# Optimization experiments

Hardware: AMD Instinct MI355X
Metric: run time of the kernel (lower is better)

Reference implementation:

```python
import jax, jax.numpy as jnp
import numpy as np

B, S, D = 2, 2048, 1024
H = 16
DH = D // H
FF = 4096
N_NEU = 4096
N_PAT = 64
K = 16          # neuron top-k
KP = 8          # pattern top-k
EPS = 1e-5


def _layer_norm(x, g, b):
    mu = jnp.mean(x, axis=-1, keepdims=True)
    var = jnp.mean((x - mu) ** 2, axis=-1, keepdims=True)
    return (x - mu) * jax.lax.rsqrt(var + EPS) * g + b


def setup_inputs() -> dict:
    key = jax.random.key(0)
    ks = jax.random.split(key, 20)
    sc = 0.02
    lin = lambda k, o, i: jax.random.normal(k, (o, i), jnp.float32) * (1.0 / np.sqrt(i))
    return {
        "x": jax.random.normal(ks[0], (B, S, D), jnp.float32),
        "neurons": jax.random.normal(ks[1], (N_NEU, D), jnp.float32) * sc,
        "wq": lin(ks[2], D, D), "bq": jnp.zeros((D,), jnp.float32),
        "wk": lin(ks[3], D, D), "bk": jnp.zeros((D,), jnp.float32),
        "wv": lin(ks[4], D, D), "bv": jnp.zeros((D,), jnp.float32),
        "wp": lin(ks[5], 2, 2 * D), "bp": jnp.zeros((2,), jnp.float32),
        "pattern_queries": jax.random.normal(ks[6], (N_PAT, D), jnp.float32) * sc,
        "gates": jax.random.normal(ks[7], (N_PAT, FF), jnp.float32) * sc,
        "w_up": lin(ks[8], FF, D), "b_up": jnp.zeros((FF,), jnp.float32),
        "w_down": lin(ks[9], D, FF), "b_down": jnp.zeros((D,), jnp.float32),
        "ln1_g": jnp.ones((D,), jnp.float32), "ln1_b": jnp.zeros((D,), jnp.float32),
        "ln2_g": jnp.ones((D,), jnp.float32), "ln2_b": jnp.zeros((D,), jnp.float32),
    }


def _forward(x, neurons, wq, bq, wk, bk, wv, bv, wp, bp, pattern_queries, gates,
             w_up, b_up, w_down, b_down, ln1_g, ln1_b, ln2_g, ln2_b):
    # ---- NeuronRouter on norm1(x) ----
    normed = _layer_norm(x, ln1_g, ln1_b)
    q = (normed @ wq.T + bq).reshape(B, S, H, DH).transpose(0, 2, 1, 3)
    k = (normed @ wk.T + bk).reshape(B, S, H, DH).transpose(0, 2, 1, 3)
    v = (normed @ wv.T + bv).reshape(B, S, H, DH).transpose(0, 2, 1, 3)
    attn = jax.nn.softmax(jnp.einsum('bhqd,bhkd->bhqk', q, k) / np.sqrt(DH), axis=-1)
    context = jnp.einsum('bhqk,bhkd->bhqd', attn, v).transpose(0, 2, 1, 3).reshape(B, S, D)

    token_scores = normed @ neurons.T                     # [B,S,N]
    context_scores = context @ neurons.T                  # [B,S,N]
    combined = jnp.concatenate([normed, context], axis=-1)
    path_w = jax.nn.softmax(combined @ wp.T + bp, axis=-1)  # [B,S,2]
    scores = path_w[..., 0:1] * token_scores + path_w[..., 1:2] * context_scores

    topk_scores, topk_idx = jax.lax.top_k(scores, K)      # [B,S,K]
    topk_weights = jax.nn.softmax(topk_scores, axis=-1)
    selected = neurons[topk_idx]                          # [B,S,K,D]
    router_out = jnp.einsum('bsk,bskd->bsd', topk_weights, selected)

    x = x + router_out

    # ---- PatternFFN on norm2(x) ----
    normed2 = _layer_norm(x, ln2_g, ln2_b)
    # similarity * neuron weight, summed over K -> pattern scores [B,S,P]
    pattern_scores = jnp.einsum('pd,bskd,bsk->bsp', pattern_queries, selected,
                                topk_weights) / np.sqrt(D)
    pat_scores, pat_idx = jax.lax.top_k(pattern_scores, KP)  # [B,S,KP]
    pat_weights = jax.nn.softmax(pat_scores, axis=-1)
    selected_gates = gates[pat_idx]                       # [B,S,KP,FF]
    ffn_gate = jnp.einsum('bsk,bskf->bsf', pat_weights, selected_gates)

    h = normed2 @ w_up.T + b_up                           # [B,S,FF]
    h = jax.nn.gelu(h * jax.nn.sigmoid(ffn_gate), approximate=False)
    ffn_out = h @ w_down.T + b_down

    return x + ffn_out, topk_idx


def reference(x, neurons, wq, bq, wk, bk, wv, bv, wp, bp, pattern_queries, gates,
              w_up, b_up, w_down, b_down, ln1_g, ln1_b, ln2_g, ln2_b):
    return _forward(x, neurons, wq, bq, wk, bk, wv, bv, wp, bp, pattern_queries,
                    gates, w_up, b_up, w_down, b_down, ln1_g, ln1_b, ln2_g, ln2_b)
```

## Files before the change

kernel.cpp:

```cpp
#include <hip/hip_runtime.h>
#include <math.h>

#define DEV static __device__ __forceinline__

constexpr int S_ = 2048;
constexpr int D_ = 1024;
constexpr int H_ = 16;

typedef __attribute__((ext_vector_type(8))) short bf16x8;
typedef __attribute__((ext_vector_type(4))) float f32x4;
typedef __attribute__((ext_vector_type(8))) short s16x8;

DEV unsigned short f2bf(float x) {
    union { float f; unsigned u; } c; c.f = x;
    const unsigned r = (c.u + 0x7FFFu + ((c.u >> 16) & 1u)) >> 16;
    return (unsigned short)r;
}
DEV float bf2f(unsigned short u) {
    union { unsigned u; float f; } c; c.u = ((unsigned)u) << 16;
    return c.f;
}

DEV float blockReduceSum(float v) {
    #pragma unroll
    for (int m = 1; m < 64; m <<= 1) v += __shfl_xor(v, m, 64);
    __shared__ float wsr[4];
    const int lane = threadIdx.x & 63, wid = threadIdx.x >> 6;
    if (lane == 0) wsr[wid] = v;
    __syncthreads();
    v = wsr[0] + wsr[1] + wsr[2] + wsr[3];
    __syncthreads();
    return v;
}

template<int BF16OUT>
__global__ __launch_bounds__(256)
void ln_k(const float* __restrict__ x, const float* __restrict__ g,
          const float* __restrict__ b, void* __restrict__ o)
{
    const int m = blockIdx.x, tid = threadIdx.x;
    const float* xr = x + (size_t)m * D_;
    const float4 xv = *(const float4*)(xr + tid * 4);
    float s = xv.x + xv.y + xv.z + xv.w;
    s = blockReduceSum(s);
    const float mu = s * (1.0f / 1024.0f);
    const float d0 = xv.x - mu, d1 = xv.y - mu, d2 = xv.z - mu, d3 = xv.w - mu;
    float sq = d0 * d0 + d1 * d1 + d2 * d2 + d3 * d3;
    sq = blockReduceSum(sq);
    const float rstd = rsqrtf(sq * (1.0f / 1024.0f) + 1e-5f);
    const float4 gv = *(const float4*)(g + tid * 4);
    const float4 bv = *(const float4*)(b + tid * 4);
    const float o0 = d0 * rstd * gv.x + bv.x;
    const float o1 = d1 * rstd * gv.y + bv.y;
    const float o2 = d2 * rstd * gv.z + bv.z;
    const float o3 = d3 * rstd * gv.w + bv.w;
    if constexpr (BF16OUT) {
        unsigned short* ob = (unsigned short*)o + (size_t)m * D_ + tid * 4;
        *(ushort4*)ob = make_ushort4(f2bf(o0), f2bf(o1), f2bf(o2), f2bf(o3));
    } else {
        *(float4*)((float*)o + (size_t)m * D_ + tid * 4) = make_float4(o0, o1, o2, o3);
    }
}

template<int MODE>
__global__ __launch_bounds__(256)
void gemm32_k(const float* __restrict__ A, const float* __restrict__ Bw,
              const float* __restrict__ bias, const float* __restrict__ extra,
              float* __restrict__ Cout, int M, int N, int Kd)
{
    __shared__ __align__(16) float As[32][132];
    __shared__ __align__(16) float Bs[32][132];
    const int tid = threadIdx.x;
    const int tx = tid & 15, ty = tid >> 4;
    const int row0 = blockIdx.y * 128, col0 = blockIdx.x * 128;
    const int lr = tid & 127, lk = (tid >> 7) * 16;
    const float* Ap = A + (size_t)(row0 + lr) * Kd + lk;
    const float* Bp = Bw + (size_t)(col0 + lr) * Kd + lk;
    float acc[8][8] = {};

    float4 ar[4], br[4];
    #pragma unroll
    for (int jj = 0; jj < 4; ++jj) {
        ar[jj] = *(const float4*)(Ap + jj * 4);
        br[jj] = *(const float4*)(Bp + jj * 4);
    }

    for (int k0 = 0; k0 < Kd; k0 += 32) {
        __syncthreads();
        #pragma unroll
        for (int jj = 0; jj < 4; ++jj) {
            As[lk + jj * 4 + 0][lr] = ar[jj].x;
            As[lk + jj * 4 + 1][lr] = ar[jj].y;
            As[lk + jj * 4 + 2][lr] = ar[jj].z;
            As[lk + jj * 4 + 3][lr] = ar[jj].w;
            Bs[lk + jj * 4 + 0][lr] = br[jj].x;
            Bs[lk + jj * 4 + 1][lr] = br[jj].y;
            Bs[lk + jj * 4 + 2][lr] = br[jj].z;
            Bs[lk + jj * 4 + 3][lr] = br[jj].w;
        }
        __syncthreads();
        if (k0 + 32 < Kd) {
            #pragma unroll
            for (int jj = 0; jj < 4; ++jj) {
                ar[jj] = *(const float4*)(Ap + k0 + 32 + jj * 4);
                br[jj] = *(const float4*)(Bp + k0 + 32 + jj * 4);
            }
        }
        #pragma unroll
        for (int kk = 0; kk < 32; ++kk) {
            float av[8], bv[8];
            *(float4*)&av[0] = *(const float4*)&As[kk][ty * 8];
            *(float4*)&av[4] = *(const float4*)&As[kk][ty * 8 + 4];
            *(float4*)&bv[0] = *(const float4*)&Bs[kk][tx * 8];
            *(float4*)&bv[4] = *(const float4*)&Bs[kk][tx * 8 + 4];
            #pragma unroll
            for (int r = 0; r < 8; ++r)
                #pragma unroll
                for (int c = 0; c < 8; ++c)
                    acc[r][c] = fmaf(av[r], bv[c], acc[r][c]);
        }
    }

    const int gr0 = row0 + ty * 8, gc0 = col0 + tx * 8;
    if constexpr (MODE == 0) {
        const int hh = gc0 >> 6, dh = gc0 & 63;
        const float4 bias0 = *(const float4*)(bias + gc0);
        const float4 bias1 = *(const float4*)(bias + gc0 + 4);
        #pragma unroll
        for (int r = 0; r < 8; ++r) {
            const int m = gr0 + r;
            const int bb = m >> 11, s = m & (S_ - 1);
            float* dst = Cout + (((size_t)(bb * H_ + hh) * S_ + s) * 64 + dh);
            *(float4*)dst = make_float4(acc[r][0] + bias0.x, acc[r][1] + bias0.y,
                                        acc[r][2] + bias0.z, acc[r][3] + bias0.w);
            *(float4*)(dst + 4) = make_float4(acc[r][4] + bias1.x, acc[r][5] + bias1.y,
                                              acc[r][6] + bias1.z, acc[r][7] + bias1.w);
        }
    } else if constexpr (MODE == 2) {
        #pragma unroll
        for (int r = 0; r < 8; ++r) {
            const float rs = extra[2 * (gr0 + r)];
            float* dst = Cout + (size_t)(gr0 + r) * N + gc0;
            *(float4*)dst = make_float4(rs * acc[r][0], rs * acc[r][1],
                                        rs * acc[r][2], rs * acc[r][3]);
            *(float4*)(dst + 4) = make_float4(rs * acc[r][4], rs * acc[r][5],
                                              rs * acc[r][6], rs * acc[r][7]);
        }
    } else {
        #pragma unroll
        for (int r = 0; r < 8; ++r) {
            const float rs = extra[2 * (gr0 + r)];
            float* dst = Cout + (size_t)(gr0 + r) * N + gc0;
            const float4 c0 = *(const float4*)dst;
            const float4 c1 = *(const float4*)(dst + 4);
            *(float4*)dst = make_float4(c0.x + rs * acc[r][0], c0.y + rs * acc[r][1],
                                        c0.z + rs * acc[r][2], c0.w + rs * acc[r][3]);
            *(float4*)(dst + 4) = make_float4(c1.x + rs * acc[r][4], c1.y + rs * acc[r][5],
                                              c1.z + rs * acc[r][6], c1.w + rs * acc[r][7]);
        }
    }
}

__global__ __launch_bounds__(256)
void attn3_k(const float* __restrict__ q, const float* __restrict__ k,
             const float* __restrict__ v, float* __restrict__ ctx)
{
    __shared__ __align__(16) float Qs[64][68];
    __shared__ __align__(16) float Ks[64][68];
    __shared__ __align__(16) float Vs[64][68];
    __shared__ __align__(16) float Ps[64][68];
    const int tid = threadIdx.x;
    const int tx = tid & 15, ty = tid >> 4;
    const int bh = blockIdx.y;
    const int q0 = blockIdx.x * 64;
    const float* qb = q + (size_t)bh * S_ * 64;
    const float* kb = k + (size_t)bh * S_ * 64;
    const float* vb = v + (size_t)bh * S_ * 64;

    const int j = tid & 63, dc = (tid >> 6) * 16;

    {
        const float* src = qb + (size_t)(q0 + j) * 64 + dc;
        const float4 t0 = *(const float4*)(src + 0);
        const float4 t1 = *(const float4*)(src + 4);
        const float4 t2 = *(const float4*)(src + 8);
        const float4 t3 = *(const float4*)(src + 12);
        Qs[dc + 0][j] = t0.x;  Qs[dc + 1][j] = t0.y;  Qs[dc + 2][j] = t0.z;  Qs[dc + 3][j] = t0.w;
        Qs[dc + 4][j] = t1.x;  Qs[dc + 5][j] = t1.y;  Qs[dc + 6][j] = t1.z;  Qs[dc + 7][j] = t1.w;
        Qs[dc + 8][j] = t2.x;  Qs[dc + 9][j] = t2.y;  Qs[dc + 10][j] = t2.z; Qs[dc + 11][j] = t2.w;
        Qs[dc + 12][j] = t3.x; Qs[dc + 13][j] = t3.y; Qs[dc + 14][j] = t3.z; Qs[dc + 15][j] = t3.w;
    }

    float4 kr0, kr1, kr2, kr3, vr0, vr1, vr2, vr3;
    {
        const float* ks = kb + (size_t)j * 64 + dc;
        const float* vs = vb + (size_t)j * 64 + dc;
        kr0 = *(const float4*)(ks + 0);  kr1 = *(const float4*)(ks + 4);
        kr2 = *(const float4*)(ks + 8);  kr3 = *(const float4*)(ks + 12);
        vr0 = *(const float4*)(vs + 0);  vr1 = *(const float4*)(vs + 4);
        vr2 = *(const float4*)(vs + 8);  vr3 = *(const float4*)(vs + 12);
    }

    float mrow[4] = {-INFINITY, -INFINITY, -INFINITY, -INFINITY};
    float lrow[4] = {0.f, 0.f, 0.f, 0.f};
    float acc[4][4] = {};

    for (int kt = 0; kt < S_; kt += 64) {
        __syncthreads();
        Ks[dc + 0][j] = kr0.x;  Ks[dc + 1][j] = kr0.y;  Ks[dc + 2][j] = kr0.z;  Ks[dc + 3][j] = kr0.w;
        Ks[dc + 4][j] = kr1.x;  Ks[dc + 5][j] = kr1.y;  Ks[dc + 6][j] = kr1.z;  Ks[dc + 7][j] = kr1.w;
        Ks[dc + 8][j] = kr2.x;  Ks[dc + 9][j] = kr2.y;  Ks[dc + 10][j] = kr2.z; Ks[dc + 11][j] = kr2.w;
        Ks[dc + 12][j] = kr3.x; Ks[dc + 13][j] = kr3.y; Ks[dc + 14][j] = kr3.z; Ks[dc + 15][j] = kr3.w;
        *(float4*)&Vs[j][dc + 0]  = vr0;
        *(float4*)&Vs[j][dc + 4]  = vr1;
        *(float4*)&Vs[j][dc + 8]  = vr2;
        *(float4*)&Vs[j][dc + 12] = vr3;
        __syncthreads();

        if (kt + 64 < S_) {
            const float* ks = kb + (size_t)(kt + 64 + j) * 64 + dc;
            const float* vs = vb + (size_t)(kt + 64 + j) * 64 + dc;
            kr0 = *(const float4*)(ks + 0);  kr1 = *(const float4*)(ks + 4);
            kr2 = *(const float4*)(ks + 8);  kr3 = *(const float4*)(ks + 12);
            vr0 = *(const float4*)(vs + 0);  vr1 = *(const float4*)(vs + 4);
            vr2 = *(const float4*)(vs + 8);  vr3 = *(const float4*)(vs + 12);
        }

        float s[4][4] = {};
        #pragma unroll 8
        for (int d = 0; d < 64; ++d) {
            const float4 q4 = *(const float4*)&Qs[d][ty * 4];
            const float4 k4 = *(const float4*)&Ks[d][tx * 4];
            s[0][0] = fmaf(q4.x, k4.x, s[0][0]); s[0][1] = fmaf(q4.x, k4.y, s[0][1]);
            s[0][2] = fmaf(q4.x, k4.z, s[0][2]); s[0][3] = fmaf(q4.x, k4.w, s[0][3]);
            s[1][0] = fmaf(q4.y, k4.x, s[1][0]); s[1][1] = fmaf(q4.y, k4.y, s[1][1]);
            s[1][2] = fmaf(q4.y, k4.z, s[1][2]); s[1][3] = fmaf(q4.y, k4.w, s[1][3]);
            s[2][0] = fmaf(q4.z, k4.x, s[2][0]); s[2][1] = fmaf(q4.z, k4.y, s[2][1]);
            s[2][2] = fmaf(q4.z, k4.z, s[2][2]); s[2][3] = fmaf(q4.z, k4.w, s[2][3]);
            s[3][0] = fmaf(q4.w, k4.x, s[3][0]); s[3][1] = fmaf(q4.w, k4.y, s[3][1]);
            s[3][2] = fmaf(q4.w, k4.z, s[3][2]); s[3][3] = fmaf(q4.w, k4.w, s[3][3]);
        }

        #pragma unroll
        for (int r = 0; r < 4; ++r) {
            float s0 = s[r][0] * 0.125f, s1 = s[r][1] * 0.125f;
            float s2 = s[r][2] * 0.125f, s3 = s[r][3] * 0.125f;
            float rm = fmaxf(fmaxf(s0, s1), fmaxf(s2, s3));
            #pragma unroll
            for (int sh = 1; sh < 16; sh <<= 1) rm = fmaxf(rm, __shfl_xor(rm, sh, 64));
            const float mn = fmaxf(mrow[r], rm);
            const float p0 = expf(s0 - mn), p1 = expf(s1 - mn);
            const float p2 = expf(s2 - mn), p3 = expf(s3 - mn);
            float rs = p0 + p1 + p2 + p3;
            #pragma unroll
            for (int sh = 1; sh < 16; sh <<= 1) rs += __shfl_xor(rs, sh, 64);
            const float esc = expf(mrow[r] - mn);
            lrow[r] = lrow[r] * esc + rs;
            mrow[r] = mn;
            acc[r][0] *= esc; acc[r][1] *= esc; acc[r][2] *= esc; acc[r][3] *= esc;
            *(float4*)&Ps[ty * 4 + r][tx * 4] = make_float4(p0, p1, p2, p3);
        }
        __syncthreads();

        #pragma unroll 4
        for (int jb = 0; jb < 16; ++jb) {
            const float4 v0 = *(const float4*)&Vs[jb * 4 + 0][tx * 4];
            const float4 v1 = *(const float4*)&Vs[jb * 4 + 1][tx * 4];
            const float4 v2 = *(const float4*)&Vs[jb * 4 + 2][tx * 4];
            const float4 v3 = *(const float4*)&Vs[jb * 4 + 3][tx * 4];
            #pragma unroll
            for (int r = 0; r < 4; ++r) {
                const float4 p4 = *(const float4*)&Ps[ty * 4 + r][jb * 4];
                acc[r][0] = fmaf(p4.x, v0.x, acc[r][0]); acc[r][1] = fmaf(p4.x, v0.y, acc[r][1]);
                acc[r][2] = fmaf(p4.x, v0.z, acc[r][2]); acc[r][3] = fmaf(p4.x, v0.w, acc[r][3]);
                acc[r][0] = fmaf(p4.y, v1.x, acc[r][0]); acc[r][1] = fmaf(p4.y, v1.y, acc[r][1]);
                acc[r][2] = fmaf(p4.y, v1.z, acc[r][2]); acc[r][3] = fmaf(p4.y, v1.w, acc[r][3]);
                acc[r][0] = fmaf(p4.z, v2.x, acc[r][0]); acc[r][1] = fmaf(p4.z, v2.y, acc[r][1]);
                acc[r][2] = fmaf(p4.z, v2.z, acc[r][2]); acc[r][3] = fmaf(p4.z, v2.w, acc[r][3]);
                acc[r][0] = fmaf(p4.w, v3.x, acc[r][0]); acc[r][1] = fmaf(p4.w, v3.y, acc[r][1]);
                acc[r][2] = fmaf(p4.w, v3.z, acc[r][2]); acc[r][3] = fmaf(p4.w, v3.w, acc[r][3]);
            }
        }
    }

    const int bb = bh >> 4, hh = bh & 15;
    #pragma unroll
    for (int r = 0; r < 4; ++r) {
        const float inv = 1.0f / lrow[r];
        *(float4*)(ctx + (size_t)(bb * S_ + q0 + ty * 4 + r) * D_ + hh * 64 + tx * 4) =
            make_float4(acc[r][0] * inv, acc[r][1] * inv, acc[r][2] * inv, acc[r][3] * inv);
    }
}

__global__ __launch_bounds__(256)
void pathw_k(const float* __restrict__ normed, const float* __restrict__ ctx,
             const float* __restrict__ wp, const float* __restrict__ bp,
             float* __restrict__ pw)
{
    const int m = blockIdx.x, tid = threadIdx.x;
    const float4 n4 = *(const float4*)(normed + (size_t)m * D_ + tid * 4);
    const float4 c4 = *(const float4*)(ctx + (size_t)m * D_ + tid * 4);
    const float4 w0n = *(const float4*)(wp + tid * 4);
    const float4 w0c = *(const float4*)(wp + 1024 + tid * 4);
    const float4 w1n = *(const float4*)(wp + 2048 + tid * 4);
    const float4 w1c = *(const float4*)(wp + 3072 + tid * 4);
    float p0 = n4.x * w0n.x + n4.y * w0n.y + n4.z * w0n.z + n4.w * w0n.w
             + c4.x * w0c.x + c4.y * w0c.y + c4.z * w0c.z + c4.w * w0c.w;
    float p1 = n4.x * w1n.x + n4.y * w1n.y + n4.z * w1n.z + n4.w * w1n.w
             + c4.x * w1c.x + c4.y * w1c.y + c4.z * w1c.z + c4.w * w1c.w;
    p0 = blockReduceSum(p0);
    p1 = blockReduceSum(p1);
    if (tid == 0) {
        const float l0 = p0 + bp[0], l1 = p1 + bp[1];
        const float mx = fmaxf(l0, l1);
        const float e0 = expf(l0 - mx), e1 = expf(l1 - mx);
        const float inv = 1.0f / (e0 + e1);
        pw[2 * m] = e0 * inv;
        pw[2 * m + 1] = e1 * inv;
    }
}

__global__ __launch_bounds__(256)
void topk_router_k(const float* __restrict__ scores, const float* __restrict__ neurons,
                   const float* __restrict__ x, float* __restrict__ idx_out,
                   float* __restrict__ x1, float* __restrict__ router)
{
    __shared__ __align__(16) float sc[4096];
    __shared__ unsigned long long wred[4];
    __shared__ int ki_s[16];
    __shared__ float kv_s[16];
    __shared__ float kw_s[16];
    const int m = blockIdx.x, tid = threadIdx.x;
    const float* srow = scores + (size_t)m * 4096;
    for (int i = tid; i < 1024; i += 256)
        *(float4*)&sc[i * 4] = *(const float4*)(srow + i * 4);
    __syncthreads();

    for (int t = 0; t < 16; ++t) {
        unsigned long long best = 0ull;
        for (int i = tid; i < 4096; i += 256) {
            unsigned u = __float_as_uint(sc[i]);
            u = (u & 0x80000000u) ? ~u : (u | 0x80000000u);
            const unsigned long long key =
                ((unsigned long long)u << 32) | (unsigned long long)(0xFFFFFFFFu - (unsigned)i);
            if (key > best) best = key;
        }
        #pragma unroll
        for (int sh = 1; sh < 64; sh <<= 1) {
            const unsigned long long o = __shfl_xor(best, sh, 64);
            if (o > best) best = o;
        }
        if ((tid & 63) == 0) wred[tid >> 6] = best;
        __syncthreads();
        if (tid == 0) {
            unsigned long long bb = wred[0];
            if (wred[1] > bb) bb = wred[1];
            if (wred[2] > bb) bb = wred[2];
            if (wred[3] > bb) bb = wred[3];
            const int idx = (int)(0xFFFFFFFFu - (unsigned)(bb & 0xFFFFFFFFull));
            ki_s[t] = idx;
            kv_s[t] = sc[idx];
            sc[idx] = -INFINITY;
        }
        __syncthreads();
    }

    if (tid == 0) {
        const float mx = kv_s[0];
        float es[16], sum = 0.f;
        #pragma unroll
        for (int t = 0; t < 16; ++t) { es[t] = expf(kv_s[t] - mx); sum += es[t]; }
        const float inv = 1.0f / sum;
        #pragma unroll
        for (int t = 0; t < 16; ++t) kw_s[t] = es[t] * inv;
    }
    __syncthreads();

    if (tid < 16) idx_out[(size_t)m * 16 + tid] = (float)ki_s[tid];

    float4 r = make_float4(0.f, 0.f, 0.f, 0.f);
    #pragma unroll
    for (int t = 0; t < 16; ++t) {
        const float w = kw_s[t];
        const float4 nv = *(const float4*)(neurons + (size_t)ki_s[t] * D_ + tid * 4);
        r.x = fmaf(w, nv.x, r.x); r.y = fmaf(w, nv.y, r.y);
        r.z = fmaf(w, nv.z, r.z); r.w = fmaf(w, nv.w, r.w);
    }
    const float4 xv = *(const float4*)(x + (size_t)m * D_ + tid * 4);
    *(float4*)(router + (size_t)m * D_ + tid * 4) = r;
    *(float4*)(x1 + (size_t)m * D_ + tid * 4) =
        make_float4(xv.x + r.x, xv.y + r.y, xv.z + r.z, xv.w + r.w);
}

__global__ __launch_bounds__(256)
void pattern_k(const float* __restrict__ router, const float* __restrict__ pq,
               const float* __restrict__ gates, unsigned short* __restrict__ gate_out)
{
    __shared__ __align__(16) float rr[1024];
    __shared__ float ps[64];
    __shared__ int pidx[8];
    __shared__ float pwt[8];
    const int m = blockIdx.x, tid = threadIdx.x;
    *(float4*)&rr[tid * 4] = *(const float4*)(router + (size_t)m * D_ + tid * 4);
    __syncthreads();

    const int p = tid >> 2, part = tid & 3;
    const float* pqr = pq + (size_t)p * D_ + part * 256;
    float sum = 0.f;
    for (int d = 0; d < 256; d += 4) {
        const float4 a = *(const float4*)(pqr + d);
        const float4 b = *(const float4*)&rr[part * 256 + d];
        sum += a.x * b.x + a.y * b.y + a.z * b.z + a.w * b.w;
    }
    sum += __shfl_xor(sum, 1, 64);
    sum += __shfl_xor(sum, 2, 64);
    if (part == 0) ps[p] = sum * (1.0f / 32.0f);
    __syncthreads();

    if (tid == 0) {
        float kv[8];
        for (int t = 0; t < 8; ++t) {
            float bv = -INFINITY; int bi = 0;
            for (int i = 0; i < 64; ++i) {
                const float vv = ps[i];
                if (vv > bv) { bv = vv; bi = i; }
            }
            kv[t] = bv; pidx[t] = bi; ps[bi] = -INFINITY;
        }
        const float mx = kv[0];
        float ee[8], tot = 0.f;
        for (int t = 0; t < 8; ++t) { ee[t] = expf(kv[t] - mx); tot += ee[t]; }
        for (int t = 0; t < 8; ++t) pwt[t] = ee[t] / tot;
    }
    __syncthreads();

    for (int f = tid * 4; f < 4096; f += 1024) {
        float4 g = make_float4(0.f, 0.f, 0.f, 0.f);
        #pragma unroll
        for (int t = 0; t < 8; ++t) {
            const float w = pwt[t];
            const float4 gv = *(const float4*)(gates + (size_t)pidx[t] * 4096 + f);
            g.x = fmaf(w, gv.x, g.x); g.y = fmaf(w, gv.y, g.y);
            g.z = fmaf(w, gv.z, g.z); g.w = fmaf(w, gv.w, g.w);
        }
        *(ushort4*)(gate_out + (size_t)m * 4096 + f) =
            make_ushort4(f2bf(g.x), f2bf(g.y), f2bf(g.z), f2bf(g.w));
    }
}

__global__ __launch_bounds__(256)
void castbf_k(const float* __restrict__ in, unsigned short* __restrict__ out, int n)
{
    const int i = (blockIdx.x * 256 + threadIdx.x) * 8;
    if (i >= n) return;
    const float4 a = *(const float4*)(in + i);
    const float4 b = *(const float4*)(in + i + 4);
    *(ushort4*)(out + i) = make_ushort4(f2bf(a.x), f2bf(a.y), f2bf(a.z), f2bf(a.w));
    *(ushort4*)(out + i + 4) = make_ushort4(f2bf(b.x), f2bf(b.y), f2bf(b.z), f2bf(b.w));
}

template<int EPI>
__global__ __launch_bounds__(256)
void gemmbf_k(const unsigned short* __restrict__ A, const unsigned short* __restrict__ Bw,
              const float* __restrict__ bias, const unsigned short* __restrict__ gate,
              const float* resid, void* Cout, int M, int N, int Kd)
{
    constexpr int LSH = 40;
    __shared__ __align__(16) unsigned short Al[128 * LSH];
    __shared__ __align__(16) unsigned short Bl[128 * LSH];
    const int tid = threadIdx.x;
    const int lane = tid & 63;
    const int w = tid >> 6, wr = w >> 1, wc = w & 1;
    const int row0 = blockIdx.y * 128, col0 = blockIdx.x * 128;

    const int o0 = tid * 16, o1 = o0 + 4096;
    const int r0 = o0 >> 6, k0e = (o0 & 63) >> 1;
    const int r1 = o1 >> 6, k1e = (o1 & 63) >> 1;
    const int l0 = r0 * LSH + k0e, l1 = r1 * LSH + k1e;
    const unsigned short* Ap0 = A + (size_t)(row0 + r0) * Kd + k0e;
    const unsigned short* Ap1 = A + (size_t)(row0 + r1) * Kd + k1e;
    const unsigned short* Bp0 = Bw + (size_t)(col0 + r0) * Kd + k0e;
    const unsigned short* Bp1 = Bw + (size_t)(col0 + r1) * Kd + k1e;

    f32x4 acc[4][4];
    #pragma unroll
    for (int m = 0; m < 4; ++m)
        #pragma unroll
        for (int n = 0; n < 4; ++n)
            #pragma unroll
            for (int e = 0; e < 4; ++e) acc[m][n][e] = 0.f;

    s16x8 ra0 = *(const s16x8*)Ap0;
    s16x8 ra1 = *(const s16x8*)Ap1;
    s16x8 rb0 = *(const s16x8*)Bp0;
    s16x8 rb1 = *(const s16x8*)Bp1;

    const int fr = lane & 15, kg = (lane >> 4) * 8;
    const unsigned short* aBase = Al + ((wr * 64 + fr) * LSH + kg);
    const unsigned short* bBase = Bl + ((wc * 64 + fr) * LSH + kg);

    for (int k0 = 0; k0 < Kd; k0 += 32) {
        __syncthreads();
        *(s16x8*)(Al + l0) = ra0;
        *(s16x8*)(Al + l1) = ra1;
        *(s16x8*)(Bl + l0) = rb0;
        *(s16x8*)(Bl + l1) = rb1;
        __syncthreads();
        if (k0 + 32 < Kd) {
            ra0 = *(const s16x8*)(Ap0 + k0 + 32);
            ra1 = *(const s16x8*)(Ap1 + k0 + 32);
            rb0 = *(const s16x8*)(Bp0 + k0 + 32);
            rb1 = *(const s16x8*)(Bp1 + k0 + 32);
        }
        bf16x8 aF[4], bF[4];
        #pragma unroll
        for (int m = 0; m < 4; ++m) aF[m] = *(const bf16x8*)(aBase + m * 16 * LSH);
        #pragma unroll
        for (int n = 0; n < 4; ++n) bF[n] = *(const bf16x8*)(bBase + n * 16 * LSH);
        #pragma unroll
        for (int m = 0; m < 4; ++m)
            #pragma unroll
            for (int n = 0; n < 4; ++n)
                acc[m][n] = __builtin_amdgcn_mfma_f32_16x16x32_bf16(aF[m], bF[n], acc[m][n], 0, 0, 0);
    }

    const int rbase = (lane >> 4) * 4;
    #pragma unroll
    for (int m = 0; m < 4; ++m) {
        #pragma unroll
        for (int n = 0; n < 4; ++n) {
            const int gcol = col0 + wc * 64 + n * 16 + (lane & 15);
            const int growb = row0 + wr * 64 + m * 16 + rbase;
            const float bc = bias[gcol];
            #pragma unroll
            for (int r = 0; r < 4; ++r) {
                const int grow = growb + r;
                const float vv = acc[m][n][r];
                if constexpr (EPI == 0) {
                    const float z = vv + bc;
                    const float gt = bf2f(gate[(size_t)grow * N + gcol]);
                    const float zz = z / (1.f + expf(-gt));
                    const float o = 0.5f * zz * (1.f + erff(zz * 0.70710678118654752440f));
                    ((unsigned short*)Cout)[(size_t)grow * N + gcol] = f2bf(o);
                } else {
                    ((float*)Cout)[(size_t)grow * N + gcol] =
                        vv + bc + resid[(size_t)grow * N + gcol];
                }
            }
        }
    }
}

extern "C" void kernel_launch(void* const* d_in, const int* in_sizes, int n_in,
                              void* d_out, int out_size, void* d_ws, size_t ws_size,
                              hipStream_t stream)
{
    const float* x      = (const float*)d_in[0];
    const float* neurons= (const float*)d_in[1];
    const float* wq = (const float*)d_in[2];  const float* bq = (const float*)d_in[3];
    const float* wk = (const float*)d_in[4];  const float* bk = (const float*)d_in[5];
    const float* wv = (const float*)d_in[6];  const float* bv = (const float*)d_in[7];
    const float* wp = (const float*)d_in[8];  const float* bp = (const float*)d_in[9];
    const float* pq = (const float*)d_in[10];
    const float* gates = (const float*)d_in[11];
    const float* w_up = (const float*)d_in[12];  const float* b_up = (const float*)d_in[13];
    const float* w_dn = (const float*)d_in[14];  const float* b_dn = (const float*)d_in[15];
    const float* ln1g = (const float*)d_in[16];  const float* ln1b = (const float*)d_in[17];
    const float* ln2g = (const float*)d_in[18];  const float* ln2b = (const float*)d_in[19];

    float* out0    = (float*)d_out;
    float* idx_out = out0 + (size_t)4096 * 1024;

    float* ws      = (float*)d_ws;
    float* scores  = ws;
    float* normed  = ws + 16777216;
    float* qb      = ws + 20971520;
    float* kb      = ws + 25165824;
    float* vb      = ws + 29360128;
    float* ctx     = ws + 33554432;
    float* router  = ws + 37748736;
    float* pw      = ws + 41943040;

    unsigned short* gate_bf   = (unsigned short*)qb;
    unsigned short* h_bf      = (unsigned short*)scores;
    unsigned short* normed2bf = (unsigned short*)(scores + 8388608);
    unsigned short* wup_bf    = (unsigned short*)router;
    unsigned short* wdn_bf    = wup_bf + 4194304;
    float* x1 = out0;

    const dim3 blk(256);

    ln_k<0><<<4096, blk, 0, stream>>>(x, ln1g, ln1b, normed);
    gemm32_k<0><<<dim3(8, 32), blk, 0, stream>>>(normed, wq, bq, nullptr, qb, 4096, 1024, 1024);
    gemm32_k<0><<<dim3(8, 32), blk, 0, stream>>>(normed, wk, bk, nullptr, kb, 4096, 1024, 1024);
    gemm32_k<0><<<dim3(8, 32), blk, 0, stream>>>(normed, wv, bv, nullptr, vb, 4096, 1024, 1024);
    attn3_k<<<dim3(32, 32), blk, 0, stream>>>(qb, kb, vb, ctx);
    pathw_k<<<4096, blk, 0, stream>>>(normed, ctx, wp, bp, pw);
    gemm32_k<2><<<dim3(32, 32), blk, 0, stream>>>(normed, neurons, nullptr, pw, scores, 4096, 4096, 1024);
    gemm32_k<3><<<dim3(32, 32), blk, 0, stream>>>(ctx, neurons, nullptr, pw + 1, scores, 4096, 4096, 1024);
    topk_router_k<<<4096, blk, 0, stream>>>(scores, neurons, x, idx_out, x1, router);
    ln_k<1><<<4096, blk, 0, stream>>>(x1, ln2g, ln2b, normed2bf);
    pattern_k<<<4096, blk, 0, stream>>>(router, pq, gates, gate_bf);
    castbf_k<<<2048, blk, 0, stream>>>(w_up, wup_bf, 4194304);
    castbf_k<<<2048, blk, 0, stream>>>(w_dn, wdn_bf, 4194304);
    gemmbf_k<0><<<dim3(32, 32), blk, 0, stream>>>(normed2bf, wup_bf, b_up, gate_bf, nullptr, h_bf, 4096, 4096, 1024);
    gemmbf_k<1><<<dim3(8, 32), blk, 0, stream>>>(h_bf, wdn_bf, b_dn, nullptr, x1, out0, 4096, 1024, 4096);
}
```

Before: 2.110 ms.

## Fuse token and context neuron-score GEMMs and alias attention P buffer

The two fp32 GEMMs computing normed@neurons^T and ctx@neurons^T are merged into one kernel that loads each neuron tile once, keeps two accumulators, and applies the path weights before a single store. This removes the second pass over the neuron matrix and the read-modify-write of the 4096x4096 score buffer. The attention kernel now reuses the K shared-memory tile for the probability matrix, cutting LDS per block at the cost of an extra barrier. The fused GEMM holds more registers per thread (64 accumulators), which may lower occupancy.

```diff
diff --git a/kernel.cpp b/kernel.cpp
--- a/kernel.cpp
+++ b/kernel.cpp
@@ -136,39 +136,105 @@
             *(float4*)(dst + 4) = make_float4(acc[r][4] + bias1.x, acc[r][5] + bias1.y,
                                               acc[r][6] + bias1.z, acc[r][7] + bias1.w);
         }
-    } else if constexpr (MODE == 2) {
-        #pragma unroll
-        for (int r = 0; r < 8; ++r) {
-            const float rs = extra[2 * (gr0 + r)];
-            float* dst = Cout + (size_t)(gr0 + r) * N + gc0;
-            *(float4*)dst = make_float4(rs * acc[r][0], rs * acc[r][1],
-                                        rs * acc[r][2], rs * acc[r][3]);
-            *(float4*)(dst + 4) = make_float4(rs * acc[r][4], rs * acc[r][5],
-                                              rs * acc[r][6], rs * acc[r][7]);
-        }
-    } else {
-        #pragma unroll
-        for (int r = 0; r < 8; ++r) {
-            const float rs = extra[2 * (gr0 + r)];
-            float* dst = Cout + (size_t)(gr0 + r) * N + gc0;
-            const float4 c0 = *(const float4*)dst;
-            const float4 c1 = *(const float4*)(dst + 4);
-            *(float4*)dst = make_float4(c0.x + rs * acc[r][0], c0.y + rs * acc[r][1],
-                                        c0.z + rs * acc[r][2], c0.w + rs * acc[r][3]);
-            *(float4*)(dst + 4) = make_float4(c1.x + rs * acc[r][4], c1.y + rs * acc[r][5],
-                                              c1.z + rs * acc[r][6], c1.w + rs * acc[r][7]);
-        }
-    }
-}
-
-__global__ __launch_bounds__(256)
-void attn3_k(const float* __restrict__ q, const float* __restrict__ k,
+    }
+}
+
+__global__ __launch_bounds__(256)
+void gemmsc_k(const float* __restrict__ A0, const float* __restrict__ A1,
+              const float* __restrict__ Bw, const float* __restrict__ pw,
+              float* __restrict__ Cout, int M, int N, int Kd)
+{
+    __shared__ __align__(16) float A0s[32][68];
+    __shared__ __align__(16) float A1s[32][68];
+    __shared__ __align__(16) float Bs[32][136];
+    const int tid = threadIdx.x;
+    const int tx = tid & 15, ty = tid >> 4;
+    const int row0 = blockIdx.y * 64, col0 = blockIdx.x * 128;
+    const int ar = tid & 63, ak = (tid >> 6) * 8;
+    const int bc = tid & 127, bk = (tid >> 7) * 16;
+    const float* A0p = A0 + (size_t)(row0 + ar) * Kd + ak;
+    const float* A1p = A1 + (size_t)(row0 + ar) * Kd + ak;
+    const float* Bp  = Bw + (size_t)(col0 + bc) * Kd + bk;
+
+    float acc0[4][8] = {}, acc1[4][8] = {};
+    float4 a0r[2], a1r[2], brr[4];
+    a0r[0] = *(const float4*)(A0p);     a0r[1] = *(const float4*)(A0p + 4);
+    a1r[0] = *(const float4*)(A1p);     a1r[1] = *(const float4*)(A1p + 4);
+    #pragma unroll
+    for (int jj = 0; jj < 4; ++jj) brr[jj] = *(const float4*)(Bp + jj * 4);
+
+    for (int k0 = 0; k0 < Kd; k0 += 32) {
+        __syncthreads();
+        #pragma unroll
+        for (int jj = 0; jj < 2; ++jj) {
+            A0s[ak + jj * 4 + 0][ar] = a0r[jj].x;
+            A0s[ak + jj * 4 + 1][ar] = a0r[jj].y;
+            A0s[ak + jj * 4 + 2][ar] = a0r[jj].z;
+            A0s[ak + jj * 4 + 3][ar] = a0r[jj].w;
+            A1s[ak + jj * 4 + 0][ar] = a1r[jj].x;
+            A1s[ak + jj * 4 + 1][ar] = a1r[jj].y;
+            A1s[ak + jj * 4 + 2][ar] = a1r[jj].z;
+            A1s[ak + jj * 4 + 3][ar] = a1r[jj].w;
+        }
+        #pragma unroll
+        for (int jj = 0; jj < 4; ++jj) {
+            Bs[bk + jj * 4 + 0][bc] = brr[jj].x;
+            Bs[bk + jj * 4 + 1][bc] = brr[jj].y;
+            Bs[bk + jj * 4 + 2][bc] = brr[jj].z;
+            Bs[bk + jj * 4 + 3][bc] = brr[jj].w;
+        }
+        __syncthreads();
+        if (k0 + 32 < Kd) {
+            a0r[0] = *(const float4*)(A0p + k0 + 32);
+            a0r[1] = *(const float4*)(A0p + k0 + 36);
+            a1r[0] = *(const float4*)(A1p + k0 + 32);
+            a1r[1] = *(const float4*)(A1p + k0 + 36);
+            #pragma unroll
+            for (int jj = 0; jj < 4; ++jj)
+                brr[jj] = *(const float4*)(Bp + k0 + 32 + jj * 4);
+        }
+        #pragma unroll
+        for (int kk = 0; kk < 32; ++kk) {
+            float av0[4], av1[4], bv[8];
+            *(float4*)&av0[0] = *(const float4*)&A0s[kk][ty * 4];
+            *(float4*)&av1[0] = *(const float4*)&A1s[kk][ty * 4];
+            *(float4*)&bv[0] = *(const float4*)&Bs[kk][tx * 8];
+            *(float4*)&bv[4] = *(const float4*)&Bs[kk][tx * 8 + 4];
+            #pragma unroll
+            for (int r = 0; r < 4; ++r)
+                #pragma unroll
+                for (int c = 0; c < 8; ++c) {
+                    acc0[r][c] = fmaf(av0[r], bv[c], acc0[r][c]);
+                    acc1[r][c] = fmaf(av1[r], bv[c], acc1[r][c]);
+                }
+        }
+    }
+
+    const int gc0 = col0 + tx * 8;
+    #pragma unroll
+    for (int r = 0; r < 4; ++r) {
+        const int grow = row0 + ty * 4 + r;
+        const float rs0 = pw[2 * grow];
+        const float rs1 = pw[2 * grow + 1];
+        float o[8];
+        #pragma unroll
+        for (int c = 0; c < 8; ++c) {
+            const float t = rs0 * acc0[r][c];
+            o[c] = t + rs1 * acc1[r][c];
+        }
+        float* dst = Cout + (size_t)grow * N + gc0;
+        *(float4*)dst = make_float4(o[0], o[1], o[2], o[3]);
+        *(float4*)(dst + 4) = make_float4(o[4], o[5], o[6], o[7]);
+    }
+}
+
+__global__ __launch_bounds__(256)
+void attn4_k(const float* __restrict__ q, const float* __restrict__ k,
              const float* __restrict__ v, float* __restrict__ ctx)
 {
     __shared__ __align__(16) float Qs[64][68];
-    __shared__ __align__(16) float Ks[64][68];
+    __shared__ __align__(16) float KP[64][68];
     __shared__ __align__(16) float Vs[64][68];
-    __shared__ __align__(16) float Ps[64][68];
     const int tid = threadIdx.x;
     const int tx = tid & 15, ty = tid >> 4;
     const int bh = blockIdx.y;
@@ -207,10 +273,10 @@
 
     for (int kt = 0; kt < S_; kt += 64) {
         __syncthreads();
-        Ks[dc + 0][j] = kr0.x;  Ks[dc + 1][j] = kr0.y;  Ks[dc + 2][j] = kr0.z;  Ks[dc + 3][j] = kr0.w;
-        Ks[dc + 4][j] = kr1.x;  Ks[dc + 5][j] = kr1.y;  Ks[dc + 6][j] = kr1.z;  Ks[dc + 7][j] = kr1.w;
-        Ks[dc + 8][j] = kr2.x;  Ks[dc + 9][j] = kr2.y;  Ks[dc + 10][j] = kr2.z; Ks[dc + 11][j] = kr2.w;
-        Ks[dc + 12][j] = kr3.x; Ks[dc + 13][j] = kr3.y; Ks[dc + 14][j] = kr3.z; Ks[dc + 15][j] = kr3.w;
+        KP[dc + 0][j] = kr0.x;  KP[dc + 1][j] = kr0.y;  KP[dc + 2][j] = kr0.z;  KP[dc + 3][j] = kr0.w;
+        KP[dc + 4][j] = kr1.x;  KP[dc + 5][j] = kr1.y;  KP[dc + 6][j] = kr1.z;  KP[dc + 7][j] = kr1.w;
+        KP[dc + 8][j] = kr2.x;  KP[dc + 9][j] = kr2.y;  KP[dc + 10][j] = kr2.z; KP[dc + 11][j] = kr2.w;
+        KP[dc + 12][j] = kr3.x; KP[dc + 13][j] = kr3.y; KP[dc + 14][j] = kr3.z; KP[dc + 15][j] = kr3.w;
         *(float4*)&Vs[j][dc + 0]  = vr0;
         *(float4*)&Vs[j][dc + 4]  = vr1;
         *(float4*)&Vs[j][dc + 8]  = vr2;
@@ -230,7 +296,7 @@
         #pragma unroll 8
         for (int d = 0; d < 64; ++d) {
             const float4 q4 = *(const float4*)&Qs[d][ty * 4];
-            const float4 k4 = *(const float4*)&Ks[d][tx * 4];
+            const float4 k4 = *(const float4*)&KP[d][tx * 4];
             s[0][0] = fmaf(q4.x, k4.x, s[0][0]); s[0][1] = fmaf(q4.x, k4.y, s[0][1]);
             s[0][2] = fmaf(q4.x, k4.z, s[0][2]); s[0][3] = fmaf(q4.x, k4.w, s[0][3]);
             s[1][0] = fmaf(q4.y, k4.x, s[1][0]); s[1][1] = fmaf(q4.y, k4.y, s[1][1]);
@@ -241,6 +307,7 @@
             s[3][2] = fmaf(q4.w, k4.z, s[3][2]); s[3][3] = fmaf(q4.w, k4.w, s[3][3]);
         }
 
+        float4 prow[4];
         #pragma unroll
         for (int r = 0; r < 4; ++r) {
             float s0 = s[r][0] * 0.125f, s1 = s[r][1] * 0.125f;
@@ -258,8 +325,12 @@
             lrow[r] = lrow[r] * esc + rs;
             mrow[r] = mn;
             acc[r][0] *= esc; acc[r][1] *= esc; acc[r][2] *= esc; acc[r][3] *= esc;
-            *(float4*)&Ps[ty * 4 + r][tx * 4] = make_float4(p0, p1, p2, p3);
-        }
+            prow[r] = make_float4(p0, p1, p2, p3);
+        }
+        __syncthreads();
+        #pragma unroll
+        for (int r = 0; r < 4; ++r)
+            *(float4*)&KP[ty * 4 + r][tx * 4] = prow[r];
         __syncthreads();
 
         #pragma unroll 4
@@ -270,7 +341,7 @@
             const float4 v3 = *(const float4*)&Vs[jb * 4 + 3][tx * 4];
             #pragma unroll
             for (int r = 0; r < 4; ++r) {
-                const float4 p4 = *(const float4*)&Ps[ty * 4 + r][jb * 4];
+                const float4 p4 = *(const float4*)&KP[ty * 4 + r][jb * 4];
                 acc[r][0] = fmaf(p4.x, v0.x, acc[r][0]); acc[r][1] = fmaf(p4.x, v0.y, acc[r][1]);
                 acc[r][2] = fmaf(p4.x, v0.z, acc[r][2]); acc[r][3] = fmaf(p4.x, v0.w, acc[r][3]);
                 acc[r][0] = fmaf(p4.y, v1.x, acc[r][0]); acc[r][1] = fmaf(p4.y, v1.y, acc[r][1]);
@@ -594,10 +665,9 @@
     gemm32_k<0><<<dim3(8, 32), blk, 0, stream>>>(normed, wq, bq, nullptr, qb, 4096, 1024, 1024);
     gemm32_k<0><<<dim3(8, 32), blk, 0, stream>>>(normed, wk, bk, nullptr, kb, 4096, 1024, 1024);
     gemm32_k<0><<<dim3(8, 32), blk, 0, stream>>>(normed, wv, bv, nullptr, vb, 4096, 1024, 1024);
-    attn3_k<<<dim3(32, 32), blk, 0, stream>>>(qb, kb, vb, ctx);
+    attn4_k<<<dim3(32, 32), blk, 0, stream>>>(qb, kb, vb, ctx);
     pathw_k<<<4096, blk, 0, stream>>>(normed, ctx, wp, bp, pw);
-    gemm32_k<2><<<dim3(32, 32), blk, 0, stream>>>(normed, neurons, nullptr, pw, scores, 4096, 4096, 1024);
-    gemm32_k<3><<<dim3(32, 32), blk, 0, stream>>>(ctx, neurons, nullptr, pw + 1, scores, 4096, 4096, 1024);
+    gemmsc_k<<<dim3(32, 64), blk, 0, stream>>>(normed, ctx, neurons, pw, scores, 4096, 4096, 1024);
     topk_router_k<<<4096, blk, 0, stream>>>(scores, neurons, x, idx_out, x1, router);
     ln_k<1><<<4096, blk, 0, stream>>>(x1, ln2g, ln2b, normed2bf);
     pattern_k<<<4096, blk, 0, stream>>>(router, pq, gates, gate_bf);
```

New measurement: 2.334 ms. +10.6%, slower.

## Enlarge attention query tile to 128 rows and add XCD-aware GEMM block swizzle

Applied to the files above, without the earlier changes.

The attention kernel now handles 128 query rows per block instead of 64, so each thread computes 8 rows. Each K/V tile loaded into shared memory is therefore reused across twice as many queries, halving K/V traffic. Separately, the fp32 and bf16 GEMMs remap workgroup IDs so that consecutive tiles land on the same XCD, aiming for better L2 locality. The cost is more registers and LDS per attention block and only 512 blocks, which may reduce occupancy.

```diff
diff --git a/kernel.cpp b/kernel.cpp
--- a/kernel.cpp
+++ b/kernel.cpp
@@ -19,6 +19,11 @@
 DEV float bf2f(unsigned short u) {
     union { unsigned u; float f; } c; c.u = ((unsigned)u) << 16;
     return c.f;
+}
+
+DEV int xcd_swizzle(int wg, int nwg) {
+    const int nx = nwg >> 3;
+    return (wg & 7) * nx + (wg >> 3);
 }
 
 DEV float blockReduceSum(float v) {
@@ -72,7 +77,10 @@
     __shared__ __align__(16) float Bs[32][132];
     const int tid = threadIdx.x;
     const int tx = tid & 15, ty = tid >> 4;
-    const int row0 = blockIdx.y * 128, col0 = blockIdx.x * 128;
+    const int swz = xcd_swizzle(blockIdx.y * gridDim.x + blockIdx.x,
+                                gridDim.x * gridDim.y);
+    const int bx = swz % gridDim.x, by = swz / gridDim.x;
+    const int row0 = by * 128, col0 = bx * 128;
     const int lr = tid & 127, lk = (tid >> 7) * 16;
     const float* Ap = A + (size_t)(row0 + lr) * Kd + lk;
     const float* Bp = Bw + (size_t)(col0 + lr) * Kd + lk;
@@ -146,7 +154,7 @@
             *(float4*)(dst + 4) = make_float4(rs * acc[r][4], rs * acc[r][5],
                                               rs * acc[r][6], rs * acc[r][7]);
         }
-    } else {
+    } else if constexpr (MODE == 3) {
         #pragma unroll
         for (int r = 0; r < 8; ++r) {
             const float rs = extra[2 * (gr0 + r)];
@@ -162,17 +170,17 @@
 }
 
 __global__ __launch_bounds__(256)
-void attn3_k(const float* __restrict__ q, const float* __restrict__ k,
+void attn5_k(const float* __restrict__ q, const float* __restrict__ k,
              const float* __restrict__ v, float* __restrict__ ctx)
 {
-    __shared__ __align__(16) float Qs[64][68];
+    __shared__ __align__(16) float Qs[64][132];
     __shared__ __align__(16) float Ks[64][68];
     __shared__ __align__(16) float Vs[64][68];
-    __shared__ __align__(16) float Ps[64][68];
+    __shared__ __align__(16) float Ps[128][68];
     const int tid = threadIdx.x;
     const int tx = tid & 15, ty = tid >> 4;
     const int bh = blockIdx.y;
-    const int q0 = blockIdx.x * 64;
+    const int q0 = blockIdx.x * 128;
     const float* qb = q + (size_t)bh * S_ * 64;
     const float* kb = k + (size_t)bh * S_ * 64;
     const float* vb = v + (size_t)bh * S_ * 64;
@@ -180,15 +188,16 @@
     const int j = tid & 63, dc = (tid >> 6) * 16;
 
     {
-        const float* src = qb + (size_t)(q0 + j) * 64 + dc;
-        const float4 t0 = *(const float4*)(src + 0);
-        const float4 t1 = *(const float4*)(src + 4);
-        const float4 t2 = *(const float4*)(src + 8);
-        const float4 t3 = *(const float4*)(src + 12);
-        Qs[dc + 0][j] = t0.x;  Qs[dc + 1][j] = t0.y;  Qs[dc + 2][j] = t0.z;  Qs[dc + 3][j] = t0.w;
-        Qs[dc + 4][j] = t1.x;  Qs[dc + 5][j] = t1.y;  Qs[dc + 6][j] = t1.z;  Qs[dc + 7][j] = t1.w;
-        Qs[dc + 8][j] = t2.x;  Qs[dc + 9][j] = t2.y;  Qs[dc + 10][j] = t2.z; Qs[dc + 11][j] = t2.w;
-        Qs[dc + 12][j] = t3.x; Qs[dc + 13][j] = t3.y; Qs[dc + 14][j] = t3.z; Qs[dc + 15][j] = t3.w;
+        const int qi = tid >> 1, qdc = (tid & 1) * 32;
+        const float* src = qb + (size_t)(q0 + qi) * 64 + qdc;
+        #pragma unroll
+        for (int u = 0; u < 8; ++u) {
+            const float4 t = *(const float4*)(src + u * 4);
+            Qs[qdc + u * 4 + 0][qi] = t.x;
+            Qs[qdc + u * 4 + 1][qi] = t.y;
+            Qs[qdc + u * 4 + 2][qi] = t.z;
+            Qs[qdc + u * 4 + 3][qi] = t.w;
+        }
     }
 
     float4 kr0, kr1, kr2, kr3, vr0, vr1, vr2, vr3;
@@ -201,9 +210,10 @@
         vr2 = *(const float4*)(vs + 8);  vr3 = *(const float4*)(vs + 12);
     }
 
-    float mrow[4] = {-INFINITY, -INFINITY, -INFINITY, -INFINITY};
-    float lrow[4] = {0.f, 0.f, 0.f, 0.f};
-    float acc[4][4] = {};
+    float mrow[8], lrow[8];
+    #pragma unroll
+    for (int r = 0; r < 8; ++r) { mrow[r] = -INFINITY; lrow[r] = 0.f; }
+    float acc[8][4] = {};
 
     for (int kt = 0; kt < S_; kt += 64) {
         __syncthreads();
@@ -226,23 +236,32 @@
             vr2 = *(const float4*)(vs + 8);  vr3 = *(const float4*)(vs + 12);
         }
 
-        float s[4][4] = {};
+        float s[8][4] = {};
         #pragma unroll 8
         for (int d = 0; d < 64; ++d) {
-            const float4 q4 = *(const float4*)&Qs[d][ty * 4];
+            const float4 qa = *(const float4*)&Qs[d][ty * 8];
+            const float4 qc = *(const float4*)&Qs[d][ty * 8 + 4];
             const float4 k4 = *(const float4*)&Ks[d][tx * 4];
-            s[0][0] = fmaf(q4.x, k4.x, s[0][0]); s[0][1] = fmaf(q4.x, k4.y, s[0][1]);
-            s[0][2] = fmaf(q4.x, k4.z, s[0][2]); s[0][3] = fmaf(q4.x, k4.w, s[0][3]);
-            s[1][0] = fmaf(q4.y, k4.x, s[1][0]); s[1][1] = fmaf(q4.y, k4.y, s[1][1]);
-            s[1][2] = fmaf(q4.y, k4.z, s[1][2]); s[1][3] = fmaf(q4.y, k4.w, s[1][3]);
-            s[2][0] = fmaf(q4.z, k4.x, s[2][0]); s[2][1] = fmaf(q4.z, k4.y, s[2][1]);
-            s[2][2] = fmaf(q4.z, k4.z, s[2][2]); s[2][3] = fmaf(q4.z, k4.w, s[2][3]);
-            s[3][0] = fmaf(q4.w, k4.x, s[3][0]); s[3][1] = fmaf(q4.w, k4.y, s[3][1]);
-            s[3][2] = fmaf(q4.w, k4.z, s[3][2]); s[3][3] = fmaf(q4.w, k4.w, s[3][3]);
-        }
-
-        #pragma unroll
-        for (int r = 0; r < 4; ++r) {
+            s[0][0] = fmaf(qa.x, k4.x, s[0][0]); s[0][1] = fmaf(qa.x, k4.y, s[0][1]);
+            s[0][2] = fmaf(qa.x, k4.z, s[0][2]); s[0][3] = fmaf(qa.x, k4.w, s[0][3]);
+            s[1][0] = fmaf(qa.y, k4.x, s[1][0]); s[1][1] = fmaf(qa.y, k4.y, s[1][1]);
+            s[1][2] = fmaf(qa.y, k4.z, s[1][2]); s[1][3] = fmaf(qa.y, k4.w, s[1][3]);
+            s[2][0] = fmaf(qa.z, k4.x, s[2][0]); s[2][1] = fmaf(qa.z, k4.y, s[2][1]);
+            s[2][2] = fmaf(qa.z, k4.z, s[2][2]); s[2][3] = fmaf(qa.z, k4.w, s[2][3]);
+            s[3][0] = fmaf(qa.w, k4.x, s[3][0]); s[3][1] = fmaf(qa.w, k4.y, s[3][1]);
+            s[3][2] = fmaf(qa.w, k4.z, s[3][2]); s[3][3] = fmaf(qa.w, k4.w, s[3][3]);
+            s[4][0] = fmaf(qc.x, k4.x, s[4][0]); s[4][1] = fmaf(qc.x, k4.y, s[4][1]);
+            s[4][2] = fmaf(qc.x, k4.z, s[4][2]); s[4][3] = fmaf(qc.x, k4.w, s[4][3]);
+            s[5][0] = fmaf(qc.y, k4.x, s[5][0]); s[5][1] = fmaf(qc.y, k4.y, s[5][1]);
+            s[5][2] = fmaf(qc.y, k4.z, s[5][2]); s[5][3] = fmaf(qc.y, k4.w, s[5][3]);
+            s[6][0] = fmaf(qc.z, k4.x, s[6][0]); s[6][1] = fmaf(qc.z, k4.y, s[6][1]);
+            s[6][2] = fmaf(qc.z, k4.z, s[6][2]); s[6][3] = fmaf(qc.z, k4.w, s[6][3]);
+            s[7][0] = fmaf(qc.w, k4.x, s[7][0]); s[7][1] = fmaf(qc.w, k4.y, s[7][1]);
+            s[7][2] = fmaf(qc.w, k4.z, s[7][2]); s[7][3] = fmaf(qc.w, k4.w, s[7][3]);
+        }
+
+        #pragma unroll
+        for (int r = 0; r < 8; ++r) {
             float s0 = s[r][0] * 0.125f, s1 = s[r][1] * 0.125f;
             float s2 = s[r][2] * 0.125f, s3 = s[r][3] * 0.125f;
             float rm = fmaxf(fmaxf(s0, s1), fmaxf(s2, s3));
@@ -258,7 +277,7 @@
             lrow[r] = lrow[r] * esc + rs;
             mrow[r] = mn;
             acc[r][0] *= esc; acc[r][1] *= esc; acc[r][2] *= esc; acc[r][3] *= esc;
-            *(float4*)&Ps[ty * 4 + r][tx * 4] = make_float4(p0, p1, p2, p3);
+            *(float4*)&Ps[ty * 8 + r][tx * 4] = make_float4(p0, p1, p2, p3);
         }
         __syncthreads();
 
@@ -269,8 +288,8 @@
             const float4 v2 = *(const float4*)&Vs[jb * 4 + 2][tx * 4];
             const float4 v3 = *(const float4*)&Vs[jb * 4 + 3][tx * 4];
             #pragma unroll
-            for (int r = 0; r < 4; ++r) {
-                const float4 p4 = *(const float4*)&Ps[ty * 4 + r][jb * 4];
+            for (int r = 0; r < 8; ++r) {
+                const float4 p4 = *(const float4*)&Ps[ty * 8 + r][jb * 4];
                 acc[r][0] = fmaf(p4.x, v0.x, acc[r][0]); acc[r][1] = fmaf(p4.x, v0.y, acc[r][1]);
                 acc[r][2] = fmaf(p4.x, v0.z, acc[r][2]); acc[r][3] = fmaf(p4.x, v0.w, acc[r][3]);
                 acc[r][0] = fmaf(p4.y, v1.x, acc[r][0]); acc[r][1] = fmaf(p4.y, v1.y, acc[r][1]);
@@ -285,9 +304,9 @@
 
     const int bb = bh >> 4, hh = bh & 15;
     #pragma unroll
-    for (int r = 0; r < 4; ++r) {
+    for (int r = 0; r < 8; ++r) {
         const float inv = 1.0f / lrow[r];
-        *(float4*)(ctx + (size_t)(bb * S_ + q0 + ty * 4 + r) * D_ + hh * 64 + tx * 4) =
+        *(float4*)(ctx + (size_t)(bb * S_ + q0 + ty * 8 + r) * D_ + hh * 64 + tx * 4) =
             make_float4(acc[r][0] * inv, acc[r][1] * inv, acc[r][2] * inv, acc[r][3] * inv);
     }
 }
@@ -471,7 +490,9 @@
     const int tid = threadIdx.x;
     const int lane = tid & 63;
     const int w = tid >> 6, wr = w >> 1, wc = w & 1;
-    const int row0 = blockIdx.y * 128, col0 = blockIdx.x * 128;
+    const int swz = xcd_swizzle(blockIdx.y * gridDim.x + blockIdx.x,
+                                gridDim.x * gridDim.y);
+    const int row0 = (swz / gridDim.x) * 128, col0 = (swz % gridDim.x) * 128;
 
     const int o0 = tid * 16, o1 = o0 + 4096;
     const int r0 = o0 >> 6, k0e = (o0 & 63) >> 1;
@@ -594,7 +615,7 @@
     gemm32_k<0><<<dim3(8, 32), blk, 0, stream>>>(normed, wq, bq, nullptr, qb, 4096, 1024, 1024);
     gemm32_k<0><<<dim3(8, 32), blk, 0, stream>>>(normed, wk, bk, nullptr, kb, 4096, 1024, 1024);
     gemm32_k<0><<<dim3(8, 32), blk, 0, stream>>>(normed, wv, bv, nullptr, vb, 4096, 1024, 1024);
-    attn3_k<<<dim3(32, 32), blk, 0, stream>>>(qb, kb, vb, ctx);
+    attn5_k<<<dim3(16, 32), blk, 0, stream>>>(qb, kb, vb, ctx);
     pathw_k<<<4096, blk, 0, stream>>>(normed, ctx, wp, bp, pw);
     gemm32_k<2><<<dim3(32, 32), blk, 0, stream>>>(normed, neurons, nullptr, pw, scores, 4096, 4096, 1024);
     gemm32_k<3><<<dim3(32, 32), blk, 0, stream>>>(ctx, neurons, nullptr, pw + 1, scores, 4096, 4096, 1024);
```

New measurement: 2.362 ms. +12.0%, slower.
